# Performance work log

Measured on AMD Instinct MI355X. Metric: run time of the kernel, lower is better.

Reference implementation:

```python
import jax, jax.numpy as jnp
import numpy as np

DIM = 1024
H_MID = max(8, DIM // 2)   # 512
H_LOW = max(8, DIM // 4)   # 256


def setup_inputs() -> dict:
    key = jax.random.key(0)
    ks = jax.random.split(key, 10)
    s = lambda fan_in: 1.0 / np.sqrt(fan_in)
    x = jax.random.normal(ks[0], (4, 8192, DIM), dtype=jnp.float32)
    return {
        "x": x,
        "gamma": jnp.ones((DIM,), jnp.float32),
        "beta": jnp.zeros((DIM,), jnp.float32),
        "W1": jax.random.uniform(ks[1], (DIM, H_MID), jnp.float32, -s(DIM), s(DIM)),
        "b1": jax.random.uniform(ks[2], (H_MID,), jnp.float32, -s(DIM), s(DIM)),
        "W2": jax.random.uniform(ks[3], (H_MID, H_MID), jnp.float32, -s(H_MID), s(H_MID)),
        "b2": jax.random.uniform(ks[4], (H_MID,), jnp.float32, -s(H_MID), s(H_MID)),
        "W3": jax.random.uniform(ks[5], (H_MID, H_LOW), jnp.float32, -s(H_MID), s(H_MID)),
        "b3": jax.random.uniform(ks[6], (H_LOW,), jnp.float32, -s(H_MID), s(H_MID)),
        "W4": jax.random.uniform(ks[7], (H_LOW, DIM), jnp.float32, -s(H_LOW), s(H_LOW)),
        "b4": jax.random.uniform(ks[8], (DIM,), jnp.float32, -s(H_LOW), s(H_LOW)),
    }


def _layernorm(x, gamma, beta, eps=1e-5):
    mu = jnp.mean(x, axis=-1, keepdims=True)
    var = jnp.mean(jnp.square(x - mu), axis=-1, keepdims=True)
    return (x - mu) * jax.lax.rsqrt(var + eps) * gamma + beta


def reference(x, gamma, beta, W1, b1, W2, b2, W3, b3, W4, b4):
    gelu = lambda h: jax.nn.gelu(h, approximate=False)  # torch default: exact erf GELU
    h = _layernorm(x, gamma, beta)                      # (B,S,D)
    h = gelu(jnp.einsum("bsd,dm->bsm", h, W1) + b1)    # (B,S,D/2)
    h = gelu(jnp.einsum("bsm,mn->bsn", h, W2) + b2)    # (B,S,D/2)
    h = gelu(jnp.einsum("bsn,nl->bsl", h, W3) + b3)    # (B,S,D/4)
    h = jnp.einsum("bsl,ld->bsd", h, W4) + b4          # (B,S,D)
    return x + h
```

## Files before the change

kernel.cpp:

```cpp
#include <hip/hip_runtime.h>


typedef short short8 __attribute__((ext_vector_type(8)));
typedef float floatx4 __attribute__((ext_vector_type(4)));
typedef unsigned short ushort4v __attribute__((ext_vector_type(4)));
typedef unsigned int uint2v __attribute__((ext_vector_type(2)));

__device__ __forceinline__ unsigned short f2bf(float f) {
    union { float f; unsigned int u; } a; a.f = f;
    unsigned int u = a.u;
    return (unsigned short)((u + 0x7FFFu + ((u >> 16) & 1u)) >> 16);
}

__device__ __forceinline__ float bf2f(unsigned short h) {
    union { unsigned int u; float f; } a; a.u = ((unsigned int)h) << 16;
    return a.f;
}

__device__ __forceinline__ unsigned int pkbf(float a, float b) {
    return (unsigned int)f2bf(a) | ((unsigned int)f2bf(b) << 16);
}

__device__ __forceinline__ float gelu_fast(float v) {
    float u = 0.7978845608f * v * (1.0f + 0.044715f * v * v);
    float e = __builtin_amdgcn_exp2f(u * 2.885390082f);
    float t = 1.0f - 2.0f * __builtin_amdgcn_rcpf(1.0f + e);
    return 0.5f * v * (1.0f + t);
}

__device__ __forceinline__ void gl_lds16(const unsigned short* g, unsigned short* l) {
    __builtin_amdgcn_global_load_lds(
        (const __attribute__((address_space(1))) void*)g,
        (__attribute__((address_space(3))) void*)l, 16, 0, 0);
}

#define BARX() asm volatile("s_barrier" ::: "memory")
#define VMW4() asm volatile("s_waitcnt vmcnt(4)" ::: "memory")
#define VMW0() asm volatile("s_waitcnt vmcnt(0)" ::: "memory")

__global__ __launch_bounds__(256) void conv_all_kernel(
    const float* __restrict__ W1, const float* __restrict__ W2,
    const float* __restrict__ W3, const float* __restrict__ W4,
    const float* __restrict__ gamma,
    unsigned short* __restrict__ Wt1, unsigned short* __restrict__ Wt2,
    unsigned short* __restrict__ Wt3, unsigned short* __restrict__ Wt4) {
    int b = blockIdx.x;
    const float* W; unsigned short* Wt; int K, N; const float* sc = nullptr;
    if (b < 2048)      { W = W1; Wt = Wt1; K = 1024; N = 512;  sc = gamma; }
    else if (b < 3072) { W = W2; Wt = Wt2; K = 512;  N = 512;  b -= 2048; }
    else if (b < 3584) { W = W3; Wt = Wt3; K = 512;  N = 256;  b -= 3072; }
    else               { W = W4; Wt = Wt4; K = 256;  N = 1024; b -= 3584; }
    int t = b * 256 + threadIdx.x;
    int sh = 31 - __clz(N);
    int k = t >> sh, n = t & (N - 1);
    float v = W[t];
    if (sc) v *= sc[k];
    Wt[(size_t)n * K + k] = f2bf(v);
}

__global__ __launch_bounds__(256) void u1c1_init_kernel(
    const float* __restrict__ b1, float* __restrict__ u1, float* __restrict__ c1,
    int N) {
    int n = blockIdx.x * 256 + threadIdx.x;
    if (n >= N) return;
    u1[n] = 0.f;
    c1[n] = b1[n];
}

__global__ __launch_bounds__(256) void u1c1_kernel(
    const float* __restrict__ W1, const float* __restrict__ gamma,
    const float* __restrict__ beta, float* __restrict__ u1,
    float* __restrict__ c1) {
    const int N = 512;
    __shared__ float gs[16], bs[16];
    int n = threadIdx.x;
    int k0 = blockIdx.x * 16;
    if (n < 16) { gs[n] = gamma[k0 + n]; bs[n] = beta[k0 + n]; }
    __syncthreads();
    float ua = 0.f, ca = 0.f, ub = 0.f, cb = 0.f;
#pragma unroll
    for (int i = 0; i < 16; i++) {
        float w0 = W1[(size_t)(k0 + i) * N + n];
        float w1 = W1[(size_t)(k0 + i) * N + n + 256];
        ua += gs[i] * w0; ca += bs[i] * w0;
        ub += gs[i] * w1; cb += bs[i] * w1;
    }
    atomicAdd(&u1[n], ua);       atomicAdd(&c1[n], ca);
    atomicAdd(&u1[n + 256], ub); atomicAdd(&c1[n + 256], cb);
}

__global__ __launch_bounds__(256) void ln_stats_kernel(
    const float* __restrict__ x, float* __restrict__ mu, float* __restrict__ rs,
    unsigned short* __restrict__ xb) {
    const int D = 1024;
    int row = blockIdx.x * 4 + (threadIdx.x >> 6);
    int lane = threadIdx.x & 63;
    const float4* xr = (const float4*)(x + (size_t)row * D);
    float s = 0.f, ss = 0.f;
#pragma unroll
    for (int i = 0; i < 4; i++) {
        float4 v = xr[lane + 64 * i];
        s  += v.x + v.y + v.z + v.w;
        ss += v.x * v.x + v.y * v.y + v.z * v.z + v.w * v.w;
        if (xb) {
            ushort4v o;
            o.x = f2bf(v.x); o.y = f2bf(v.y); o.z = f2bf(v.z); o.w = f2bf(v.w);
            *(ushort4v*)(xb + (size_t)row * D + 4 * (lane + 64 * i)) = o;
        }
    }
#pragma unroll
    for (int off = 32; off; off >>= 1) {
        s  += __shfl_xor(s, off);
        ss += __shfl_xor(ss, off);
    }
    if (lane == 0) {
        float m = s * (1.0f / 1024.0f);
        mu[row] = m;
        rs[row] = rsqrtf(ss * (1.0f / 1024.0f) - m * m + 1e-5f);
    }
}

__device__ __forceinline__ void ldA8(const unsigned short* base, short8 (&a)[8]) {
#pragma unroll
    for (int mt = 0; mt < 8; mt++) a[mt] = *(const short8*)(base + mt * 512);
}
__device__ __forceinline__ void ldB2(const unsigned short* base, short8 (&bb)[2]) {
    bb[0] = *(const short8*)(base);
    bb[1] = *(const short8*)(base + 512);
}
template <int CH>
__device__ __forceinline__ void mm16(const short8 (&a)[8], const short8 (&bb)[2],
                                     floatx4 (&acc)[8][4]) {
    __builtin_amdgcn_s_setprio(1);
#pragma unroll
    for (int mt = 0; mt < 8; mt++)
#pragma unroll
        for (int nt = 0; nt < 2; nt++)
            acc[mt][CH * 2 + nt] = __builtin_amdgcn_mfma_f32_16x16x32_bf16(
                bb[nt], a[mt], acc[mt][CH * 2 + nt], 0, 0, 0);
    __builtin_amdgcn_s_setprio(0);
}

template <int KLEN, bool PF>
__device__ __forceinline__ void do_tile(
    const unsigned short* aK0, const unsigned short* aK1,
    const unsigned short* bK0, const unsigned short* bK1,
    unsigned short* stA0, unsigned short* stA1,
    unsigned short* stB0, unsigned short* stB1,
    const unsigned short* gAs, const unsigned short* gBs,
    short8 (&a)[8], short8 (&bb)[2], floatx4 (&acc)[8][4]) {
    ldA8(aK0, a);
    ldB2(bK0, bb);
    if (PF) {
        gl_lds16(gAs, stA0);
        gl_lds16(gAs + (size_t)128 * KLEN, stA0 + 4096);
    }
    mm16<0>(a, bb, acc);
    BARX();
    ldB2(bK0 + 1024, bb);
    if (PF) {
        gl_lds16(gBs, stB0);
        gl_lds16(gBs + (size_t)128 * KLEN, stB0 + 4096);
    }
    mm16<1>(a, bb, acc);
    if (PF) { VMW4(); } else { VMW0(); }
    BARX();
    ldA8(aK1, a);
    ldB2(bK1, bb);
    if (PF) {
        gl_lds16(gAs + 32, stA1);
        gl_lds16(gAs + 32 + (size_t)128 * KLEN, stA1 + 4096);
    }
    mm16<0>(a, bb, acc);
    BARX();
    ldB2(bK1 + 1024, bb);
    if (PF) {
        gl_lds16(gBs + 32, stB1);
        gl_lds16(gBs + 32 + (size_t)128 * KLEN, stB1 + 4096);
    }
    mm16<1>(a, bb, acc);
    if (PF) { VMW4(); }
    BARX();
}

template <int EPMODE, int NBN, int NT, int NOUT, int KLEN>
__global__ __launch_bounds__(512, 2) void gemm256_kernel(
    const unsigned short* __restrict__ A, const unsigned short* __restrict__ Bt,
    unsigned short* __restrict__ Out,
    const float* __restrict__ bias,
    const float* __restrict__ u1,
    const float* __restrict__ mu,
    const float* __restrict__ rs)
{
    __shared__ unsigned short lds[2][2][2][8192];

    const int tid  = threadIdx.x;
    const int wave = tid >> 6;
    const int lane = tid & 63;
    const int q    = lane >> 4;
    const int l16  = lane & 15;
    const int wm   = wave >> 2;
    const int wn   = wave & 3;

    const int id   = blockIdx.x;
    const int xcd  = id & 7;
    const int slot = id >> 3;
    const int m0   = (xcd + 8 * (slot / NBN)) * 256;
    const int n0   = (slot % NBN) * 256;

    const unsigned short* gAs = A  + (size_t)(m0 + (tid >> 2)) * KLEN + (tid & 3) * 8;
    const unsigned short* gBs = Bt + (size_t)(n0 + (tid >> 2)) * KLEN + (tid & 3) * 8;

    const int wo = wave << 9;
    unsigned short* stA00 = &lds[0][0][0][0] + wo;
    unsigned short* stA01 = &lds[0][0][1][0] + wo;
    unsigned short* stB00 = &lds[0][1][0][0] + wo;
    unsigned short* stB01 = &lds[0][1][1][0] + wo;
    unsigned short* stA10 = &lds[1][0][0][0] + wo;
    unsigned short* stA11 = &lds[1][0][1][0] + wo;
    unsigned short* stB10 = &lds[1][1][0][0] + wo;
    unsigned short* stB11 = &lds[1][1][1][0] + wo;

    const int aoff = (wm * 128 + l16) * 32 + q * 8;
    const int boff = (wn * 64 + l16) * 32 + q * 8;
    const unsigned short* aF00 = &lds[0][0][0][0] + aoff;
    const unsigned short* aF01 = &lds[0][0][1][0] + aoff;
    const unsigned short* bF00 = &lds[0][1][0][0] + boff;
    const unsigned short* bF01 = &lds[0][1][1][0] + boff;
    const unsigned short* aF10 = &lds[1][0][0][0] + aoff;
    const unsigned short* aF11 = &lds[1][0][1][0] + aoff;
    const unsigned short* bF10 = &lds[1][1][0][0] + boff;
    const unsigned short* bF11 = &lds[1][1][1][0] + boff;

    floatx4 acc[8][4] = {};
    short8 a[8], bb[2];

    gl_lds16(gAs,                           stA00);
    gl_lds16(gAs + (size_t)128 * KLEN,      stA00 + 4096);
    gl_lds16(gBs,                           stB00);
    gl_lds16(gBs + (size_t)128 * KLEN,      stB00 + 4096);
    gl_lds16(gAs + 32,                      stA01);
    gl_lds16(gAs + 32 + (size_t)128 * KLEN, stA01 + 4096);
    gl_lds16(gBs + 32,                      stB01);
    gl_lds16(gBs + 32 + (size_t)128 * KLEN, stB01 + 4096);
    VMW4();
    BARX();
    gAs += 64; gBs += 64;

    for (int t = 0; t + 2 < NT; t += 2) {
        do_tile<KLEN, true>(aF00, aF01, bF00, bF01, stA10, stA11, stB10, stB11,
                            gAs, gBs, a, bb, acc);
        gAs += 64; gBs += 64;
        do_tile<KLEN, true>(aF10, aF11, bF10, bF11, stA00, stA01, stB00, stB01,
                            gAs, gBs, a, bb, acc);
        gAs += 64; gBs += 64;
    }
    do_tile<KLEN, true>(aF00, aF01, bF00, bF01, stA10, stA11, stB10, stB11,
                        gAs, gBs, a, bb, acc);
    do_tile<KLEN, false>(aF10, aF11, bF10, bF11, stA00, stA01, stB00, stB01,
                         gAs, gBs, a, bb, acc);

    float rs8[8], mu8[8];
    if constexpr (EPMODE == 0) {
#pragma unroll
        for (int ma = 0; ma < 8; ma++) {
            const int row = m0 + wm * 128 + ma * 16 + l16;
            rs8[ma] = rs[row];
            mu8[ma] = mu[row];
        }
    }
#pragma unroll
    for (int na = 0; na < 4; na++) {
        const int nb = n0 + wn * 64 + na * 16 + q * 4;
        const float4 bv = *(const float4*)(bias + nb);
        float4 uv = {0.f, 0.f, 0.f, 0.f};
        if constexpr (EPMODE == 0) uv = *(const float4*)(u1 + nb);
#pragma unroll
        for (int ma = 0; ma < 8; ma++) {
            const int row = m0 + wm * 128 + ma * 16 + l16;
            const size_t off = (size_t)row * NOUT + nb;
            float v0 = acc[ma][na][0], v1 = acc[ma][na][1];
            float v2 = acc[ma][na][2], v3 = acc[ma][na][3];
            if constexpr (EPMODE == 0) {
                v0 = gelu_fast(rs8[ma] * (v0 - mu8[ma] * uv.x) + bv.x);
                v1 = gelu_fast(rs8[ma] * (v1 - mu8[ma] * uv.y) + bv.y);
                v2 = gelu_fast(rs8[ma] * (v2 - mu8[ma] * uv.z) + bv.z);
                v3 = gelu_fast(rs8[ma] * (v3 - mu8[ma] * uv.w) + bv.w);
            } else {
                v0 = gelu_fast(v0 + bv.x);
                v1 = gelu_fast(v1 + bv.y);
                v2 = gelu_fast(v2 + bv.z);
                v3 = gelu_fast(v3 + bv.w);
            }
            uint2v o; o.x = pkbf(v0, v1); o.y = pkbf(v2, v3);
            *(uint2v*)(Out + off) = o;
        }
    }
}

template <int EPMODE, bool AF32, int NBN, int NT_, int KT>
__global__ __launch_bounds__(256) void gemm_kernel(
    const void* __restrict__ Aptr, const unsigned short* __restrict__ Bt,
    void* __restrict__ Out,
    const float* __restrict__ bias,
    const float* __restrict__ u1,
    const float* __restrict__ mu,
    const float* __restrict__ rs,
    const void* __restrict__ resid)
{
    constexpr int BM = 128, BN = 128, BK = 64;
    constexpr int N = NT_, K = KT;
    __shared__ unsigned short As[BM][BK];
    __shared__ unsigned short Bs[BN][BK];

    const int tid  = threadIdx.x;
    const int wave = tid >> 6;
    const int lane = tid & 63;
    const int q    = lane >> 4;
    const int l16  = lane & 15;
    const int wm   = wave & 1;
    const int wn   = wave >> 1;

    const int id   = blockIdx.x;
    const int xcd  = id & 7;
    const int slot = id >> 3;
    const int m0   = (xcd + 8 * (slot / NBN)) * BM;
    const int n0   = (slot % NBN) * BN;

    const int sr  = tid >> 3;
    const int sc  = tid & 7;
    const int sg  = sc ^ (sr & 7);
    unsigned short* lA = &As[0][0] + (wave << 9);
    unsigned short* lB = &Bs[0][0] + (wave << 9);
    const unsigned short* gb0 = Bt + (size_t)(n0 + sr) * K + sg * 8;
    const unsigned short* ga0 = nullptr;
    if (!AF32) ga0 = (const unsigned short*)Aptr + (size_t)(m0 + sr) * K + sg * 8;

    floatx4 acc[4][4] = {};

#pragma unroll
    for (int k0 = 0; k0 < K; k0 += BK) {
        if (AF32) {
            const float* A = (const float*)Aptr;
            int c = tid & 15, r0 = tid >> 4;
#pragma unroll
            for (int i = 0; i < 8; i++) {
                int r = r0 + 16 * i;
                float4 v = *(const float4*)(A + (size_t)(m0 + r) * K + k0 + c * 4);
                ushort4v o;
                o.x = f2bf(v.x); o.y = f2bf(v.y);
                o.z = f2bf(v.z); o.w = f2bf(v.w);
                int idx = r * 64 + (((c >> 1) ^ (r & 7)) << 3) + ((c & 1) << 2);
                *(ushort4v*)(&As[0][0] + idx) = o;
            }
        } else {
#pragma unroll
            for (int c = 0; c < 4; c++)
                gl_lds16(ga0 + k0 + (size_t)(32 * c) * K, lA + c * 2048);
        }
#pragma unroll
        for (int c = 0; c < 4; c++)
            gl_lds16(gb0 + k0 + (size_t)(32 * c) * K, lB + c * 2048);
        __syncthreads();

#pragma unroll
        for (int kk = 0; kk < 2; kk++) {
            const int gsw = ((kk * 4 + q) ^ (l16 & 7)) * 8;
            short8 a[4], b[4];
#pragma unroll
            for (int mt = 0; mt < 4; mt++)
                a[mt] = *(const short8*)(&As[0][0] + (wm * 64 + mt * 16 + l16) * 64 + gsw);
#pragma unroll
            for (int nt = 0; nt < 4; nt++)
                b[nt] = *(const short8*)(&Bs[0][0] + (wn * 64 + nt * 16 + l16) * 64 + gsw);
#pragma unroll
            for (int nt = 0; nt < 4; nt++)
#pragma unroll
                for (int mt = 0; mt < 4; mt++)
                    acc[nt][mt] = __builtin_amdgcn_mfma_f32_16x16x32_bf16(
                        b[nt], a[mt], acc[nt][mt], 0, 0, 0);
        }
        __syncthreads();
    }

    float rs4[4], mu4[4];
    if constexpr (EPMODE == 0) {
#pragma unroll
        for (int mt = 0; mt < 4; mt++) {
            const int row = m0 + wm * 64 + mt * 16 + l16;
            rs4[mt] = rs[row];
            mu4[mt] = mu[row];
        }
    }
#pragma unroll
    for (int nt = 0; nt < 4; nt++) {
        const int nbase = n0 + wn * 64 + nt * 16 + q * 4;
        const float4 bv = *(const float4*)(bias + nbase);
        float4 uv = {0.f, 0.f, 0.f, 0.f};
        if constexpr (EPMODE == 0) uv = *(const float4*)(u1 + nbase);
#pragma unroll
        for (int mt = 0; mt < 4; mt++) {
            const int row = m0 + wm * 64 + mt * 16 + l16;
            const size_t off = (size_t)row * N + nbase;
            float v0 = acc[nt][mt][0], v1 = acc[nt][mt][1];
            float v2 = acc[nt][mt][2], v3 = acc[nt][mt][3];
            if constexpr (EPMODE == 0) {
                v0 = gelu_fast(rs4[mt] * (v0 - mu4[mt] * uv.x) + bv.x);
                v1 = gelu_fast(rs4[mt] * (v1 - mu4[mt] * uv.y) + bv.y);
                v2 = gelu_fast(rs4[mt] * (v2 - mu4[mt] * uv.z) + bv.z);
                v3 = gelu_fast(rs4[mt] * (v3 - mu4[mt] * uv.w) + bv.w);
                uint2v o; o.x = pkbf(v0, v1); o.y = pkbf(v2, v3);
                *(uint2v*)((unsigned short*)Out + off) = o;
            } else if constexpr (EPMODE == 1) {
                v0 = gelu_fast(v0 + bv.x);
                v1 = gelu_fast(v1 + bv.y);
                v2 = gelu_fast(v2 + bv.z);
                v3 = gelu_fast(v3 + bv.w);
                uint2v o; o.x = pkbf(v0, v1); o.y = pkbf(v2, v3);
                *(uint2v*)((unsigned short*)Out + off) = o;
            } else if constexpr (EPMODE == 2) {
                const float4 rv = *(const float4*)((const float*)resid + off);
                float4 o;
                o.x = v0 + bv.x + rv.x;
                o.y = v1 + bv.y + rv.y;
                o.z = v2 + bv.z + rv.z;
                o.w = v3 + bv.w + rv.w;
                *(float4*)((float*)Out + off) = o;
            } else {
                const ushort4v rv =
                    *(const ushort4v*)((const unsigned short*)resid + off);
                float4 o;
                o.x = v0 + bv.x + bf2f(rv.x);
                o.y = v1 + bv.y + bf2f(rv.y);
                o.z = v2 + bv.z + bf2f(rv.z);
                o.w = v3 + bv.w + bf2f(rv.w);
                *(float4*)((float*)Out + off) = o;
            }
        }
    }
}

extern "C" void kernel_launch(void* const* d_in, const int* in_sizes, int n_in,
                              void* d_out, int out_size, void* d_ws, size_t ws_size,
                              hipStream_t stream) {
    const float* x     = (const float*)d_in[0];
    const float* gamma = (const float*)d_in[1];
    const float* beta  = (const float*)d_in[2];
    const float* W1    = (const float*)d_in[3];
    const float* b1    = (const float*)d_in[4];
    const float* W2    = (const float*)d_in[5];
    const float* b2    = (const float*)d_in[6];
    const float* W3    = (const float*)d_in[7];
    const float* b3    = (const float*)d_in[8];
    const float* W4    = (const float*)d_in[9];
    const float* b4    = (const float*)d_in[10];
    float* out = (float*)d_out;

    const int D = 1024, H1 = 512, H2 = 512;
    const int M = in_sizes[0] / D;

    char* ws = (char*)d_ws;
    unsigned short* Wt1 = (unsigned short*)(ws + 0);
    unsigned short* Wt2 = (unsigned short*)(ws + 1048576);
    unsigned short* Wt3 = (unsigned short*)(ws + 1572864);
    unsigned short* Wt4 = (unsigned short*)(ws + 1835008);
    float* u1           = (float*)(ws + 2359296);
    float* c1           = (float*)(ws + 2361344);
    float* muv          = (float*)(ws + 2363392);
    float* rsv          = (float*)(ws + 2494464);
    unsigned short* h1  = (unsigned short*)(ws + 2625536);
    unsigned short* h2  = (unsigned short*)(ws + 36179968);
    unsigned short* h3  = h1;
    size_t base_end     = 36179968 + (size_t)M * H2 * 2;
    unsigned short* xb  = (unsigned short*)(ws + base_end);
    bool use_xb = (ws_size >= base_end + (size_t)M * D * 2);

    const int NBM = M / 128;

    conv_all_kernel<<<4608, 256, 0, stream>>>(W1, W2, W3, W4, gamma,
                                              Wt1, Wt2, Wt3, Wt4);
    u1c1_init_kernel<<<(H1 + 255) / 256, 256, 0, stream>>>(b1, u1, c1, H1);
    u1c1_kernel<<<D / 16, 256, 0, stream>>>(W1, gamma, beta, u1, c1);

    ln_stats_kernel<<<M / 4, 256, 0, stream>>>(x, muv, rsv, use_xb ? xb : nullptr);

    if (use_xb) {
        gemm256_kernel<0, 2, 16, 512, 1024><<<(M / 256) * 2, 512, 0, stream>>>(
            xb, Wt1, h1, c1, u1, muv, rsv);
    } else {
        gemm_kernel<0, true, 4, 512, 1024><<<4 * NBM, 256, 0, stream>>>(
            x, Wt1, h1, c1, u1, muv, rsv, nullptr);
    }
    gemm256_kernel<1, 2, 8, 512, 512><<<(M / 256) * 2, 512, 0, stream>>>(
        h1, Wt2, h2, b2, nullptr, nullptr, nullptr);
    gemm_kernel<1, false, 2, 256, 512><<<2 * NBM, 256, 0, stream>>>(
        h2, Wt3, h3, b3, nullptr, nullptr, nullptr, nullptr);
    if (use_xb) {
        gemm_kernel<3, false, 8, 1024, 256><<<8 * NBM, 256, 0, stream>>>(
            h3, Wt4, out, b4, nullptr, nullptr, nullptr, xb);
    } else {
        gemm_kernel<2, false, 8, 1024, 256><<<8 * NBM, 256, 0, stream>>>(
            h3, Wt4, out, b4, nullptr, nullptr, nullptr, x);
    }
}
```

Baseline: 398.3 us.

## Deepen GEMM LDS pipeline to four stages and fold u1/c1 init into conversion

The 256x256 GEMM kernel now uses a 4-slot rotating LDS ring instead of a 2x2 double buffer. It prefetches three K-chunks ahead and waits with vmcnt(8), so more global-to-LDS loads stay in flight during MFMA work. The u1/c1 initialization is merged into the weight-conversion kernel as two extra blocks, which removes one launch. LDS use per block stays the same, but the deeper prefetch and reworked tail modes add risk around ordering and barrier correctness.

```diff
diff --git a/kernel.cpp b/kernel.cpp
--- a/kernel.cpp
+++ b/kernel.cpp
@@ -35,16 +35,24 @@
 }
 
 #define BARX() asm volatile("s_barrier" ::: "memory")
+#define VMW8() asm volatile("s_waitcnt vmcnt(8)" ::: "memory")
 #define VMW4() asm volatile("s_waitcnt vmcnt(4)" ::: "memory")
 #define VMW0() asm volatile("s_waitcnt vmcnt(0)" ::: "memory")
 
 __global__ __launch_bounds__(256) void conv_all_kernel(
     const float* __restrict__ W1, const float* __restrict__ W2,
     const float* __restrict__ W3, const float* __restrict__ W4,
-    const float* __restrict__ gamma,
+    const float* __restrict__ gamma, const float* __restrict__ b1,
     unsigned short* __restrict__ Wt1, unsigned short* __restrict__ Wt2,
-    unsigned short* __restrict__ Wt3, unsigned short* __restrict__ Wt4) {
+    unsigned short* __restrict__ Wt3, unsigned short* __restrict__ Wt4,
+    float* __restrict__ u1, float* __restrict__ c1) {
     int b = blockIdx.x;
+    if (b >= 4608) {
+        int n = (b - 4608) * 256 + threadIdx.x;
+        u1[n] = 0.f;
+        c1[n] = b1[n];
+        return;
+    }
     const float* W; unsigned short* Wt; int K, N; const float* sc = nullptr;
     if (b < 2048)      { W = W1; Wt = Wt1; K = 1024; N = 512;  sc = gamma; }
     else if (b < 3072) { W = W2; Wt = Wt2; K = 512;  N = 512;  b -= 2048; }
@@ -58,15 +66,6 @@
     Wt[(size_t)n * K + k] = f2bf(v);
 }
 
-__global__ __launch_bounds__(256) void u1c1_init_kernel(
-    const float* __restrict__ b1, float* __restrict__ u1, float* __restrict__ c1,
-    int N) {
-    int n = blockIdx.x * 256 + threadIdx.x;
-    if (n >= N) return;
-    u1[n] = 0.f;
-    c1[n] = b1[n];
-}
-
 __global__ __launch_bounds__(256) void u1c1_kernel(
     const float* __restrict__ W1, const float* __restrict__ gamma,
     const float* __restrict__ beta, float* __restrict__ u1,
@@ -141,45 +140,46 @@
     __builtin_amdgcn_s_setprio(0);
 }
 
-template <int KLEN, bool PF>
+template <int KLEN, int MODE>
 __device__ __forceinline__ void do_tile(
-    const unsigned short* aK0, const unsigned short* aK1,
-    const unsigned short* bK0, const unsigned short* bK1,
-    unsigned short* stA0, unsigned short* stA1,
-    unsigned short* stB0, unsigned short* stB1,
+    const unsigned short* aF0, const unsigned short* bF0,
+    const unsigned short* aF1, const unsigned short* bF1,
+    unsigned short* sA3, unsigned short* sB3,
+    unsigned short* sA4, unsigned short* sB4,
     const unsigned short* gAs, const unsigned short* gBs,
     short8 (&a)[8], short8 (&bb)[2], floatx4 (&acc)[8][4]) {
-    ldA8(aK0, a);
-    ldB2(bK0, bb);
-    if (PF) {
-        gl_lds16(gAs, stA0);
-        gl_lds16(gAs + (size_t)128 * KLEN, stA0 + 4096);
+    ldA8(aF0, a);
+    ldB2(bF0, bb);
+    if (MODE <= 1) {
+        gl_lds16(gAs + 96, sA3);
+        gl_lds16(gAs + 96 + (size_t)128 * KLEN, sA3 + 4096);
     }
     mm16<0>(a, bb, acc);
     BARX();
-    ldB2(bK0 + 1024, bb);
-    if (PF) {
-        gl_lds16(gBs, stB0);
-        gl_lds16(gBs + (size_t)128 * KLEN, stB0 + 4096);
+    ldB2(bF0 + 1024, bb);
+    if (MODE <= 1) {
+        gl_lds16(gBs + 96, sB3);
+        gl_lds16(gBs + 96 + (size_t)128 * KLEN, sB3 + 4096);
     }
     mm16<1>(a, bb, acc);
-    if (PF) { VMW4(); } else { VMW0(); }
+    if (MODE <= 1) { VMW8(); } else { VMW0(); }
     BARX();
-    ldA8(aK1, a);
-    ldB2(bK1, bb);
-    if (PF) {
-        gl_lds16(gAs + 32, stA1);
-        gl_lds16(gAs + 32 + (size_t)128 * KLEN, stA1 + 4096);
+    ldA8(aF1, a);
+    ldB2(bF1, bb);
+    if (MODE == 0) {
+        gl_lds16(gAs + 128, sA4);
+        gl_lds16(gAs + 128 + (size_t)128 * KLEN, sA4 + 4096);
     }
     mm16<0>(a, bb, acc);
     BARX();
-    ldB2(bK1 + 1024, bb);
-    if (PF) {
-        gl_lds16(gBs + 32, stB1);
-        gl_lds16(gBs + 32 + (size_t)128 * KLEN, stB1 + 4096);
+    ldB2(bF1 + 1024, bb);
+    if (MODE == 0) {
+        gl_lds16(gBs + 128, sB4);
+        gl_lds16(gBs + 128 + (size_t)128 * KLEN, sB4 + 4096);
     }
     mm16<1>(a, bb, acc);
-    if (PF) { VMW4(); }
+    if (MODE == 0) { VMW8(); }
+    else if (MODE == 1) { VMW4(); }
     BARX();
 }
 
@@ -192,7 +192,7 @@
     const float* __restrict__ mu,
     const float* __restrict__ rs)
 {
-    __shared__ unsigned short lds[2][2][2][8192];
+    __shared__ unsigned short lds[4][2][8192];
 
     const int tid  = threadIdx.x;
     const int wave = tid >> 6;
@@ -212,53 +212,43 @@
     const unsigned short* gBs = Bt + (size_t)(n0 + (tid >> 2)) * KLEN + (tid & 3) * 8;
 
     const int wo = wave << 9;
-    unsigned short* stA00 = &lds[0][0][0][0] + wo;
-    unsigned short* stA01 = &lds[0][0][1][0] + wo;
-    unsigned short* stB00 = &lds[0][1][0][0] + wo;
-    unsigned short* stB01 = &lds[0][1][1][0] + wo;
-    unsigned short* stA10 = &lds[1][0][0][0] + wo;
-    unsigned short* stA11 = &lds[1][0][1][0] + wo;
-    unsigned short* stB10 = &lds[1][1][0][0] + wo;
-    unsigned short* stB11 = &lds[1][1][1][0] + wo;
-
+    unsigned short* sA[4]; unsigned short* sB[4];
+    const unsigned short* fA[4]; const unsigned short* fB[4];
     const int aoff = (wm * 128 + l16) * 32 + q * 8;
     const int boff = (wn * 64 + l16) * 32 + q * 8;
-    const unsigned short* aF00 = &lds[0][0][0][0] + aoff;
-    const unsigned short* aF01 = &lds[0][0][1][0] + aoff;
-    const unsigned short* bF00 = &lds[0][1][0][0] + boff;
-    const unsigned short* bF01 = &lds[0][1][1][0] + boff;
-    const unsigned short* aF10 = &lds[1][0][0][0] + aoff;
-    const unsigned short* aF11 = &lds[1][0][1][0] + aoff;
-    const unsigned short* bF10 = &lds[1][1][0][0] + boff;
-    const unsigned short* bF11 = &lds[1][1][1][0] + boff;
+#pragma unroll
+    for (int s = 0; s < 4; s++) {
+        sA[s] = &lds[s][0][0] + wo;
+        sB[s] = &lds[s][1][0] + wo;
+        fA[s] = &lds[s][0][0] + aoff;
+        fB[s] = &lds[s][1][0] + boff;
+    }
 
     floatx4 acc[8][4] = {};
     short8 a[8], bb[2];
 
-    gl_lds16(gAs,                           stA00);
-    gl_lds16(gAs + (size_t)128 * KLEN,      stA00 + 4096);
-    gl_lds16(gBs,                           stB00);
-    gl_lds16(gBs + (size_t)128 * KLEN,      stB00 + 4096);
-    gl_lds16(gAs + 32,                      stA01);
-    gl_lds16(gAs + 32 + (size_t)128 * KLEN, stA01 + 4096);
-    gl_lds16(gBs + 32,                      stB01);
-    gl_lds16(gBs + 32 + (size_t)128 * KLEN, stB01 + 4096);
-    VMW4();
+    gl_lds16(gAs,      sA[0]); gl_lds16(gAs      + (size_t)128 * KLEN, sA[0] + 4096);
+    gl_lds16(gBs,      sB[0]); gl_lds16(gBs      + (size_t)128 * KLEN, sB[0] + 4096);
+    gl_lds16(gAs + 32, sA[1]); gl_lds16(gAs + 32 + (size_t)128 * KLEN, sA[1] + 4096);
+    gl_lds16(gBs + 32, sB[1]); gl_lds16(gBs + 32 + (size_t)128 * KLEN, sB[1] + 4096);
+    gl_lds16(gAs + 64, sA[2]); gl_lds16(gAs + 64 + (size_t)128 * KLEN, sA[2] + 4096);
+    gl_lds16(gBs + 64, sB[2]); gl_lds16(gBs + 64 + (size_t)128 * KLEN, sB[2] + 4096);
+    VMW8();
     BARX();
+
+    for (int t = 0; t + 2 < NT; t += 2) {
+        do_tile<KLEN, 0>(fA[0], fB[0], fA[1], fB[1], sA[3], sB[3], sA[0], sB[0],
+                         gAs, gBs, a, bb, acc);
+        gAs += 64; gBs += 64;
+        do_tile<KLEN, 0>(fA[2], fB[2], fA[3], fB[3], sA[1], sB[1], sA[2], sB[2],
+                         gAs, gBs, a, bb, acc);
+        gAs += 64; gBs += 64;
+    }
+    do_tile<KLEN, 1>(fA[0], fB[0], fA[1], fB[1], sA[3], sB[3], sA[0], sB[0],
+                     gAs, gBs, a, bb, acc);
     gAs += 64; gBs += 64;
-
-    for (int t = 0; t + 2 < NT; t += 2) {
-        do_tile<KLEN, true>(aF00, aF01, bF00, bF01, stA10, stA11, stB10, stB11,
-                            gAs, gBs, a, bb, acc);
-        gAs += 64; gBs += 64;
-        do_tile<KLEN, true>(aF10, aF11, bF10, bF11, stA00, stA01, stB00, stB01,
-                            gAs, gBs, a, bb, acc);
-        gAs += 64; gBs += 64;
-    }
-    do_tile<KLEN, true>(aF00, aF01, bF00, bF01, stA10, stA11, stB10, stB11,
-                        gAs, gBs, a, bb, acc);
-    do_tile<KLEN, false>(aF10, aF11, bF10, bF11, stA00, stA01, stB00, stB01,
-                         gAs, gBs, a, bb, acc);
+    do_tile<KLEN, 2>(fA[2], fB[2], fA[3], fB[3], sA[1], sB[1], sA[2], sB[2],
+                     gAs, gBs, a, bb, acc);
 
     float rs8[8], mu8[8];
     if constexpr (EPMODE == 0) {
@@ -477,9 +467,8 @@
 
     const int NBM = M / 128;
 
-    conv_all_kernel<<<4608, 256, 0, stream>>>(W1, W2, W3, W4, gamma,
-                                              Wt1, Wt2, Wt3, Wt4);
-    u1c1_init_kernel<<<(H1 + 255) / 256, 256, 0, stream>>>(b1, u1, c1, H1);
+    conv_all_kernel<<<4610, 256, 0, stream>>>(W1, W2, W3, W4, gamma, b1,
+                                              Wt1, Wt2, Wt3, Wt4, u1, c1);
     u1c1_kernel<<<D / 16, 256, 0, stream>>>(W1, gamma, beta, u1, c1);
 
     ln_stats_kernel<<<M / 4, 256, 0, stream>>>(x, muv, rsv, use_xb ? xb : nullptr);
```

Measured after the change: 399.0 us. Within noise of the previous version (+0.2%).
